# Optimization experiments

Measured on AMD Instinct MI355X. Metric: run time of the kernel, lower is better.

Reference implementation:

```python
import jax, jax.numpy as jnp
import numpy as np

B, T_OBS, T_FUT, D, H = 8192, 128, 64, 5, 128


def _gru_step(h, x, Wih, Whh, bih, bhh):
    # PyTorch GRU math, gate order (r, z, n) in the stacked [3H, *] weights.
    gi = x @ Wih.T + bih          # [B, 3H]
    gh = h @ Whh.T + bhh          # [B, 3H]
    ir, iz, inn = jnp.split(gi, 3, axis=-1)
    hr, hz, hn = jnp.split(gh, 3, axis=-1)
    r = jax.nn.sigmoid(ir + hr)
    z = jax.nn.sigmoid(iz + hz)
    n = jnp.tanh(inn + r * hn)
    return (1.0 - z) * n + z * h


def setup_inputs() -> dict:
    key = jax.random.key(0)
    ks = jax.random.split(key, 12)
    s = 0.1  # modest init scale to keep gates in a sane range
    return {
        "obs": jax.random.normal(ks[0], (B, T_OBS, D), jnp.float32),
        "target": jax.random.normal(ks[1], (B, T_FUT, D), jnp.float32),
        "enc_Wih": jax.random.normal(ks[2], (3 * H, D), jnp.float32) * s,
        "enc_Whh": jax.random.normal(ks[3], (3 * H, H), jnp.float32) * s,
        "enc_bih": jax.random.normal(ks[4], (3 * H,), jnp.float32) * s,
        "enc_bhh": jax.random.normal(ks[5], (3 * H,), jnp.float32) * s,
        "cell_Wih": jax.random.normal(ks[6], (3 * H, D), jnp.float32) * s,
        "cell_Whh": jax.random.normal(ks[7], (3 * H, H), jnp.float32) * s,
        "cell_bih": jax.random.normal(ks[8], (3 * H,), jnp.float32) * s,
        "cell_bhh": jax.random.normal(ks[9], (3 * H,), jnp.float32) * s,
        "head_W": jax.random.normal(ks[10], (D, H), jnp.float32) * s,
        "head_b": jax.random.normal(ks[11], (D,), jnp.float32) * s,
    }


def reference(obs, target, enc_Wih, enc_Whh, enc_bih, enc_bhh,
              cell_Wih, cell_Whh, cell_bih, cell_bhh, head_W, head_b):
    b = obs.shape[0]
    h0 = jnp.zeros((b, H), obs.dtype)

    # --- encoder: GRU over obs, keep only final hidden state ---
    def enc_step(h, x):
        h_new = _gru_step(h, x, enc_Wih, enc_Whh, enc_bih, enc_bhh)
        return h_new, None
    hT, _ = jax.lax.scan(enc_step, h0, jnp.swapaxes(obs, 0, 1))  # xs: [T_obs, B, D]

    # --- teacher-forced rollout: x_0 = obs[:, -1], x_t = target[:, t-1] ---
    xs = jnp.concatenate([obs[:, -1:, :], target[:, :-1, :]], axis=1)  # [B, T_fut, D]
    def roll_step(h, x):
        h_new = _gru_step(h, x, cell_Wih, cell_Whh, cell_bih, cell_bhh)
        return h_new, h_new
    _, hs = jax.lax.scan(roll_step, hT, jnp.swapaxes(xs, 0, 1))  # hs: [T_fut, B, H]

    preds = jnp.einsum('tbh,dh->tbd', hs, head_W) + head_b  # [T_fut, B, D]
    return jnp.swapaxes(preds, 0, 1)  # [B, T_fut, D]
```

## Files before the change

### kernel.cpp

```cpp
#include <hip/hip_runtime.h>

#define B_TOT 8192
#define T_OBS 128
#define T_FUT 64
#define T_ALL 192
#define DIN 5
#define HD 128
#define BT 32
#define LDSTR 136

typedef __attribute__((ext_vector_type(8))) short short8;
typedef __attribute__((ext_vector_type(4))) float f32x4;

__device__ inline short f2bf(float f) {
    unsigned u = __float_as_uint(f);
    u += 0x7FFFu + ((u >> 16) & 1u);
    return (short)(u >> 16);
}

__device__ inline float sigm(float x) {
    return __builtin_amdgcn_rcpf(1.f + __expf(-x));
}
__device__ inline float tanh_(float x) {
    return 1.f - 2.f * __builtin_amdgcn_rcpf(1.f + __expf(2.f * x));
}

__device__ inline f32x4 MFMA(short8 a, short8 b, f32x4 c) {
    return __builtin_amdgcn_mfma_f32_16x16x32_bf16(a, b, c, 0, 0, 0);
}

__device__ inline short8 load_w8(const float* p) {
    float4 a = *reinterpret_cast<const float4*>(p);
    float4 b = *reinterpret_cast<const float4*>(p + 4);
    short8 r;
    r[0] = f2bf(a.x); r[1] = f2bf(a.y); r[2] = f2bf(a.z); r[3] = f2bf(a.w);
    r[4] = f2bf(b.x); r[5] = f2bf(b.y); r[6] = f2bf(b.z); r[7] = f2bf(b.w);
    return r;
}
__device__ inline short8 load_w5(const float* p) {
    short8 r = (short8)0;
    r[0] = f2bf(p[0]); r[1] = f2bf(p[1]); r[2] = f2bf(p[2]);
    r[3] = f2bf(p[3]); r[4] = f2bf(p[4]);
    return r;
}

__global__ __launch_bounds__(512, 2)
void gru_tracemodel_kernel(const float* __restrict__ obs, const float* __restrict__ target,
                           const float* __restrict__ eWih, const float* __restrict__ eWhh,
                           const float* __restrict__ ebih, const float* __restrict__ ebhh,
                           const float* __restrict__ cWih, const float* __restrict__ cWhh,
                           const float* __restrict__ cbih, const float* __restrict__ cbhh,
                           const float* __restrict__ headW, const float* __restrict__ headb,
                           float* __restrict__ out)
{
    __shared__ __attribute__((aligned(16))) short Abuf[2][BT][LDSTR];

    const int tid   = threadIdx.x;
    const int wave  = tid >> 6;
    const int lane  = tid & 63;
    const int q     = lane >> 4;
    const int c     = lane & 15;
    const int b0    = blockIdx.x * BT;
    const int wbase = wave * 16;

    for (int i = tid; i < 2 * BT * LDSTR; i += 512) ((short*)Abuf)[i] = 0;

    short8 Wr[5], Wz[5], Wn[5];
    float  br, bz, bnh_, bni_;

    auto load_phase = [&](const float* Wih, const float* Whh,
                          const float* bih, const float* bhh) {
        const int nr = 0 * HD + wbase + c;
        const int nz = 1 * HD + wbase + c;
        const int nn = 2 * HD + wbase + c;
        #pragma unroll
        for (int kt = 0; kt < 4; ++kt) {
            Wr[kt] = load_w8(Whh + nr * HD + kt * 32 + q * 8);
            Wz[kt] = load_w8(Whh + nz * HD + kt * 32 + q * 8);
            Wn[kt] = load_w8(Whh + nn * HD + kt * 32 + q * 8);
        }
        Wr[4] = (q == 0) ? load_w5(Wih + nr * DIN) : (short8)0;
        Wz[4] = (q == 0) ? load_w5(Wih + nz * DIN) : (short8)0;
        Wn[4] = (q == 0) ? load_w5(Wih + nn * DIN) : (short8)0;
        br   = bih[nr] + bhh[nr];
        bz   = bih[nz] + bhh[nz];
        bnh_ = bhh[nn];
        bni_ = bih[nn];
    };
    load_phase(eWih, eWhh, ebih, ebhh);

    short8 Whd[4];
    float  hb = 0.f;
    if (wave == 0) {
        #pragma unroll
        for (int kt = 0; kt < 4; ++kt)
            Whd[kt] = (c < DIN) ? load_w8(headW + c * HD + kt * 32 + q * 8) : (short8)0;
        hb = (c < DIN) ? headb[c] : 0.f;
    }

    float hreg[2][4] = {{0.f,0.f,0.f,0.f},{0.f,0.f,0.f,0.f}};

    const float* obsr[2] = { obs + (size_t)(b0 + c) * (T_OBS * DIN),
                             obs + (size_t)(b0 + 16 + c) * (T_OBS * DIN) };
    const float* tgtr[2] = { target + (size_t)(b0 + c) * (T_FUT * DIN),
                             target + (size_t)(b0 + 16 + c) * (T_FUT * DIN) };
    float x5[2][5] = {{0,0,0,0,0},{0,0,0,0,0}};
    if (q == 0) {
        #pragma unroll
        for (int a = 0; a < 2; ++a)
            #pragma unroll
            for (int j = 0; j < DIN; ++j) x5[a][j] = obsr[a][j];
    }

    for (int t = 0; t <= T_ALL; ++t) {
        __syncthreads();
        const int p = t & 1;

        short8 ah[2][4];
        #pragma unroll
        for (int a = 0; a < 2; ++a) {
            const short* ap = &Abuf[p][a * 16 + c][0];
            #pragma unroll
            for (int kt = 0; kt < 4; ++kt)
                ah[a][kt] = *reinterpret_cast<const short8*>(ap + kt * 32 + q * 8);
        }

        if (wave == 0 && t >= T_OBS + 1) {
            const int s = t - (T_OBS + 1);
            #pragma unroll
            for (int a = 0; a < 2; ++a) {
                f32x4 acc = {hb, hb, hb, hb};
                #pragma unroll
                for (int kt = 0; kt < 4; ++kt)
                    acc = MFMA(ah[a][kt], Whd[kt], acc);
                if (c < DIN) {
                    #pragma unroll
                    for (int r = 0; r < 4; ++r) {
                        int m = a * 16 + q * 4 + r;
                        out[((size_t)(b0 + m) * T_FUT + s) * DIN + c] = acc[r];
                    }
                }
            }
        }
        if (t == T_ALL) break;

        if (t == T_OBS) load_phase(cWih, cWhh, cbih, cbhh);

        short8 ax[2] = {(short8)0, (short8)0};
        if (q == 0) {
            #pragma unroll
            for (int a = 0; a < 2; ++a)
                #pragma unroll
                for (int j = 0; j < DIN; ++j) ax[a][j] = f2bf(x5[a][j]);
            const int tn = t + 1;
            if (tn < T_ALL) {
                #pragma unroll
                for (int a = 0; a < 2; ++a) {
                    const float* px = (tn < T_OBS)  ? (obsr[a] + tn * DIN)
                                    : (tn == T_OBS) ? (obsr[a] + (T_OBS - 1) * DIN)
                                                    : (tgtr[a] + (tn - T_OBS - 1) * DIN);
                    #pragma unroll
                    for (int j = 0; j < DIN; ++j) x5[a][j] = px[j];
                }
            }
        }

        f32x4 aR[2], aZ[2], aNh[2], aNi[2];
        #pragma unroll
        for (int a = 0; a < 2; ++a) {
            aR[a]  = {br, br, br, br};
            aZ[a]  = {bz, bz, bz, bz};
            aNh[a] = {bnh_, bnh_, bnh_, bnh_};
            aNi[a] = {bni_, bni_, bni_, bni_};
            #pragma unroll
            for (int kt = 0; kt < 4; ++kt) {
                aR[a]  = MFMA(ah[a][kt], Wr[kt], aR[a]);
                aZ[a]  = MFMA(ah[a][kt], Wz[kt], aZ[a]);
                aNh[a] = MFMA(ah[a][kt], Wn[kt], aNh[a]);
            }
            aR[a]  = MFMA(ax[a], Wr[4], aR[a]);
            aZ[a]  = MFMA(ax[a], Wz[4], aZ[a]);
            aNi[a] = MFMA(ax[a], Wn[4], aNi[a]);
        }

        #pragma unroll
        for (int a = 0; a < 2; ++a)
            #pragma unroll
            for (int r = 0; r < 4; ++r) {
                float rv = sigm(aR[a][r]);
                float zv = sigm(aZ[a][r]);
                float nv = tanh_(aNi[a][r] + rv * aNh[a][r]);
                float hn = nv + zv * (hreg[a][r] - nv);
                hreg[a][r] = hn;
                Abuf[1 - p][a * 16 + q * 4 + r][wbase + c] = f2bf(hn);
            }
    }
}

extern "C" void kernel_launch(void* const* d_in, const int* in_sizes, int n_in,
                              void* d_out, int out_size, void* d_ws, size_t ws_size,
                              hipStream_t stream)
{
    (void)in_sizes; (void)n_in; (void)d_ws; (void)ws_size; (void)out_size;
    gru_tracemodel_kernel<<<dim3(B_TOT / BT), dim3(512), 0, stream>>>(
        (const float*)d_in[0],  (const float*)d_in[1],
        (const float*)d_in[2],  (const float*)d_in[3],
        (const float*)d_in[4],  (const float*)d_in[5],
        (const float*)d_in[6],  (const float*)d_in[7],
        (const float*)d_in[8],  (const float*)d_in[9],
        (const float*)d_in[10], (const float*)d_in[11],
        (float*)d_out);
}
```

Measured before the change: 401.9 us.

## Halve batch tile per block and stage GRU inputs and head weights in LDS

```diff
diff --git a/kernel.cpp b/kernel.cpp
--- a/kernel.cpp
+++ b/kernel.cpp
@@ -6,7 +6,7 @@
 #define T_ALL 192
 #define DIN 5
 #define HD 128
-#define BT 32
+#define BT 16
 #define LDSTR 136
 
 typedef __attribute__((ext_vector_type(8))) short short8;
@@ -44,7 +44,7 @@
     return r;
 }
 
-__global__ __launch_bounds__(512, 2)
+__global__ __launch_bounds__(512, 4)
 void gru_tracemodel_kernel(const float* __restrict__ obs, const float* __restrict__ target,
                            const float* __restrict__ eWih, const float* __restrict__ eWhh,
                            const float* __restrict__ ebih, const float* __restrict__ ebhh,
@@ -54,6 +54,8 @@
                            float* __restrict__ out)
 {
     __shared__ __attribute__((aligned(16))) short Abuf[2][BT][LDSTR];
+    __shared__ __attribute__((aligned(16))) short Xbuf[T_ALL][BT][8];
+    __shared__ __attribute__((aligned(16))) short HeadLds[4][64][8];
 
     const int tid   = threadIdx.x;
     const int wave  = tid >> 6;
@@ -63,7 +65,20 @@
     const int b0    = blockIdx.x * BT;
     const int wbase = wave * 16;
 
-    for (int i = tid; i < 2 * BT * LDSTR; i += 512) ((short*)Abuf)[i] = 0;
+    for (int i = tid; i < BT * LDSTR; i += 512) ((short*)Abuf)[i] = 0;
+
+    for (int i = tid; i < T_ALL * BT; i += 512) {
+        const int t = i % T_ALL;
+        const int r = i / T_ALL;
+        const float* src;
+        if (t < T_OBS)       src = obs    + ((size_t)(b0 + r) * T_OBS + t) * DIN;
+        else if (t == T_OBS) src = obs    + ((size_t)(b0 + r) * T_OBS + (T_OBS - 1)) * DIN;
+        else                 src = target + ((size_t)(b0 + r) * T_FUT + (t - T_OBS - 1)) * DIN;
+        short* dst = &Xbuf[t][r][0];
+        #pragma unroll
+        for (int j = 0; j < DIN; ++j) dst[j] = f2bf(src[j]);
+        dst[5] = 0; dst[6] = 0; dst[7] = 0;
+    }
 
     short8 Wr[5], Wz[5], Wn[5];
     float  br, bz, bnh_, bni_;
@@ -89,111 +104,73 @@
     };
     load_phase(eWih, eWhh, ebih, ebhh);
 
-    short8 Whd[4];
-    float  hb = 0.f;
+    float hb = 0.f;
     if (wave == 0) {
         #pragma unroll
-        for (int kt = 0; kt < 4; ++kt)
-            Whd[kt] = (c < DIN) ? load_w8(headW + c * HD + kt * 32 + q * 8) : (short8)0;
+        for (int kt = 0; kt < 4; ++kt) {
+            short8 w = (c < DIN) ? load_w8(headW + c * HD + kt * 32 + q * 8) : (short8)0;
+            *reinterpret_cast<short8*>(&HeadLds[kt][lane][0]) = w;
+        }
         hb = (c < DIN) ? headb[c] : 0.f;
     }
 
-    float hreg[2][4] = {{0.f,0.f,0.f,0.f},{0.f,0.f,0.f,0.f}};
-
-    const float* obsr[2] = { obs + (size_t)(b0 + c) * (T_OBS * DIN),
-                             obs + (size_t)(b0 + 16 + c) * (T_OBS * DIN) };
-    const float* tgtr[2] = { target + (size_t)(b0 + c) * (T_FUT * DIN),
-                             target + (size_t)(b0 + 16 + c) * (T_FUT * DIN) };
-    float x5[2][5] = {{0,0,0,0,0},{0,0,0,0,0}};
-    if (q == 0) {
-        #pragma unroll
-        for (int a = 0; a < 2; ++a)
-            #pragma unroll
-            for (int j = 0; j < DIN; ++j) x5[a][j] = obsr[a][j];
-    }
+    float hreg[4] = {0.f, 0.f, 0.f, 0.f};
 
     for (int t = 0; t <= T_ALL; ++t) {
         __syncthreads();
         const int p = t & 1;
 
-        short8 ah[2][4];
+        short8 ah[4];
+        const short* ap = &Abuf[p][c][0];
         #pragma unroll
-        for (int a = 0; a < 2; ++a) {
-            const short* ap = &Abuf[p][a * 16 + c][0];
-            #pragma unroll
-            for (int kt = 0; kt < 4; ++kt)
-                ah[a][kt] = *reinterpret_cast<const short8*>(ap + kt * 32 + q * 8);
-        }
+        for (int kt = 0; kt < 4; ++kt)
+            ah[kt] = *reinterpret_cast<const short8*>(ap + kt * 32 + q * 8);
 
         if (wave == 0 && t >= T_OBS + 1) {
             const int s = t - (T_OBS + 1);
+            f32x4 acc = {hb, hb, hb, hb};
             #pragma unroll
-            for (int a = 0; a < 2; ++a) {
-                f32x4 acc = {hb, hb, hb, hb};
+            for (int kt = 0; kt < 4; ++kt)
+                acc = MFMA(ah[kt],
+                           *reinterpret_cast<const short8*>(&HeadLds[kt][lane][0]),
+                           acc);
+            if (c < DIN) {
                 #pragma unroll
-                for (int kt = 0; kt < 4; ++kt)
-                    acc = MFMA(ah[a][kt], Whd[kt], acc);
-                if (c < DIN) {
-                    #pragma unroll
-                    for (int r = 0; r < 4; ++r) {
-                        int m = a * 16 + q * 4 + r;
-                        out[((size_t)(b0 + m) * T_FUT + s) * DIN + c] = acc[r];
-                    }
-                }
+                for (int r = 0; r < 4; ++r)
+                    out[((size_t)(b0 + q * 4 + r) * T_FUT + s) * DIN + c] = acc[r];
             }
         }
         if (t == T_ALL) break;
 
         if (t == T_OBS) load_phase(cWih, cWhh, cbih, cbhh);
 
-        short8 ax[2] = {(short8)0, (short8)0};
-        if (q == 0) {
-            #pragma unroll
-            for (int a = 0; a < 2; ++a)
-                #pragma unroll
-                for (int j = 0; j < DIN; ++j) ax[a][j] = f2bf(x5[a][j]);
-            const int tn = t + 1;
-            if (tn < T_ALL) {
-                #pragma unroll
-                for (int a = 0; a < 2; ++a) {
-                    const float* px = (tn < T_OBS)  ? (obsr[a] + tn * DIN)
-                                    : (tn == T_OBS) ? (obsr[a] + (T_OBS - 1) * DIN)
-                                                    : (tgtr[a] + (tn - T_OBS - 1) * DIN);
-                    #pragma unroll
-                    for (int j = 0; j < DIN; ++j) x5[a][j] = px[j];
-                }
-            }
+        short8 ax = (short8)0;
+        if (q == 0)
+            ax = *reinterpret_cast<const short8*>(&Xbuf[t][c][0]);
+
+        f32x4 aR  = {br, br, br, br};
+        f32x4 aZ  = {bz, bz, bz, bz};
+        f32x4 aNh = {bnh_, bnh_, bnh_, bnh_};
+        f32x4 aNi = {bni_, bni_, bni_, bni_};
+        #pragma unroll
+        for (int kt = 0; kt < 4; ++kt) {
+            aR  = MFMA(ah[kt], Wr[kt], aR);
+            aZ  = MFMA(ah[kt], Wz[kt], aZ);
+            aNh = MFMA(ah[kt], Wn[kt], aNh);
         }
-
-        f32x4 aR[2], aZ[2], aNh[2], aNi[2];
-        #pragma unroll
-        for (int a = 0; a < 2; ++a) {
-            aR[a]  = {br, br, br, br};
-            aZ[a]  = {bz, bz, bz, bz};
-            aNh[a] = {bnh_, bnh_, bnh_, bnh_};
-            aNi[a] = {bni_, bni_, bni_, bni_};
-            #pragma unroll
-            for (int kt = 0; kt < 4; ++kt) {
-                aR[a]  = MFMA(ah[a][kt], Wr[kt], aR[a]);
-                aZ[a]  = MFMA(ah[a][kt], Wz[kt], aZ[a]);
-                aNh[a] = MFMA(ah[a][kt], Wn[kt], aNh[a]);
-            }
-            aR[a]  = MFMA(ax[a], Wr[4], aR[a]);
-            aZ[a]  = MFMA(ax[a], Wz[4], aZ[a]);
-            aNi[a] = MFMA(ax[a], Wn[4], aNi[a]);
-        }
+        aR  = MFMA(ax, Wr[4], aR);
+        aZ  = MFMA(ax, Wz[4], aZ);
+        aNi = MFMA(ax, Wn[4], aNi);
 
         #pragma unroll
-        for (int a = 0; a < 2; ++a)
-            #pragma unroll
-            for (int r = 0; r < 4; ++r) {
-                float rv = sigm(aR[a][r]);
-                float zv = sigm(aZ[a][r]);
-                float nv = tanh_(aNi[a][r] + rv * aNh[a][r]);
-                float hn = nv + zv * (hreg[a][r] - nv);
-                hreg[a][r] = hn;
-                Abuf[1 - p][a * 16 + q * 4 + r][wbase + c] = f2bf(hn);
-            }
+        for (int r = 0; r < 4; ++r) {
+            float rv = sigm(aR[r]);
+            float zv = sigm(aZ[r]);
+            float nv = tanh_(aNi[r] + rv * aNh[r]);
+            float hn = nv + zv * (hreg[r] - nv);
+            hreg[r] = hn;
+            Abuf[1 - p][q * 4 + r][wbase + c] = f2bf(hn);
+        }
     }
 }
 
```

New measurement: 544.1 us. 1.35x slower.
